# Optimization experiments

Hardware: AMD Instinct MI355X
Metric: run time of the kernel (lower is better)

The kernel has to match this reference:

```python
import jax, jax.numpy as jnp
import numpy as np

N = 10000
E = 320000


def spmm(edge_row, edge_col, edge_val, h):
    # out[i] = sum_{e: row[e]==i} val[e] * h[col[e]]  (sparse adjacency @ h)
    msgs = edge_val[:, None] * h[edge_col]          # [E, d]
    return jax.ops.segment_sum(msgs, edge_row, num_segments=N)


def setup_inputs() -> dict:
    key = jax.random.key(0)
    ks = jax.random.split(key, 8)
    x = jax.random.normal(ks[0], (N, 128), dtype=jnp.float32)
    edge_row = jax.random.randint(ks[1], (E,), 0, N, dtype=jnp.int32)
    edge_col = jax.random.randint(ks[2], (E,), 0, N, dtype=jnp.int32)
    edge_val = jax.random.uniform(ks[3], (E,), dtype=jnp.float32)
    # Xavier-uniform-ish init as in the torch module: U(-1/sqrt(fan_out), 1/sqrt(fan_out))
    def w(k, fi, fo):
        s = 1.0 / np.sqrt(fo)
        return jax.random.uniform(k, (fi, fo), minval=-s, maxval=s, dtype=jnp.float32)
    W0 = w(ks[4], 128, 128)
    W1 = w(ks[5], 128, 128)
    W2 = w(ks[6], 128, 64)
    Wb = w(ks[7], 64, 64)
    return {"x": x, "edge_row": edge_row, "edge_col": edge_col, "edge_val": edge_val,
            "W0": W0, "W1": W1, "W2": W2, "Wb": Wb}


def reference(x, edge_row, edge_col, edge_val, W0, W1, W2, Wb):
    h = x
    for W in (W0, W1, W2):
        h = jax.nn.elu(spmm(edge_row, edge_col, edge_val, h @ W))
        # dropout is inactive in eval mode (training=False)
    S = (Wb + Wb.T) * 0.5                          # symmetric [d, d]
    out = jax.nn.sigmoid(h @ (S @ h.T))            # [N, N]
    return out
```

## Files before the change

### kernel.cpp

```cpp
#include <hip/hip_runtime.h>
#include <hip/hip_bf16.h>
#include <math.h>

typedef short short8 __attribute__((ext_vector_type(8)));
typedef short short4v __attribute__((ext_vector_type(4)));
typedef float f32x4 __attribute__((ext_vector_type(4)));

__device__ inline void bsplit(float x, short& h, short& l) {
    __hip_bfloat16 hb = __float2bfloat16(x);
    float hf = __bfloat162float(hb);
    __hip_bfloat16 lb = __float2bfloat16(x - hf);
    h = *reinterpret_cast<short*>(&hb);
    l = *reinterpret_cast<short*>(&lb);
}


__global__ void zero_i32(int* __restrict__ p, int n) {
    int i = blockIdx.x * blockDim.x + threadIdx.x;
    if (i < n) p[i] = 0;
}

__global__ void hist_kernel(const int* __restrict__ row, int* __restrict__ hist, int E) {
    int i = blockIdx.x * blockDim.x + threadIdx.x;
    if (i < E) atomicAdd(&hist[row[i]], 1);
}

__global__ void scan_kernel(const int* __restrict__ hist, int* __restrict__ rowptr,
                            int* __restrict__ cursor, int n) {
    __shared__ int wsum[16];
    __shared__ int carry_s;
    int tid = threadIdx.x, lane = tid & 63, wid = tid >> 6;
    if (tid == 0) { carry_s = 0; rowptr[0] = 0; }
    __syncthreads();
    for (int base = 0; base < n; base += 1024) {
        int idx = base + tid;
        int v = (idx < n) ? hist[idx] : 0;
        int x = v;
#pragma unroll
        for (int d = 1; d < 64; d <<= 1) {
            int t = __shfl_up(x, d, 64);
            if (lane >= d) x += t;
        }
        if (lane == 63) wsum[wid] = x;
        __syncthreads();
        if (wid == 0) {
            int s = (lane < 16) ? wsum[lane] : 0;
#pragma unroll
            for (int d = 1; d < 16; d <<= 1) {
                int t = __shfl_up(s, d, 64);
                if (lane >= d) s += t;
            }
            if (lane < 16) wsum[lane] = s;
        }
        __syncthreads();
        int woff = (wid > 0) ? wsum[wid - 1] : 0;
        int inc = x + woff + carry_s;
        if (idx < n) {
            rowptr[idx + 1] = inc;
            cursor[idx] = inc - v;
        }
        __syncthreads();
        if (tid == 1023) carry_s = inc;
        __syncthreads();
    }
}

__global__ void scatter_kernel(const int* __restrict__ row, const int* __restrict__ col,
                               const float* __restrict__ val, int* __restrict__ cursor,
                               int* __restrict__ colsort, float* __restrict__ valsort, int E) {
    int i = blockIdx.x * blockDim.x + threadIdx.x;
    if (i < E) {
        int r = row[i];
        int p = atomicAdd(&cursor[r], 1);
        colsort[p] = col[i];
        valsort[p] = val[i];
    }
}

template <int K, int M>
__global__ void gemm_layer(const float* __restrict__ A, const float* __restrict__ W,
                           float* __restrict__ out, int n) {
    __shared__ float a[8 * K];
    int j = threadIdx.x;
    int row0 = blockIdx.x * 8;
    constexpr int K4 = K / 4;
    for (int idx = j; idx < 8 * K4; idx += M) {
        int r = idx / K4, k4 = idx % K4;
        float4 v = make_float4(0.f, 0.f, 0.f, 0.f);
        if (row0 + r < n) v = *reinterpret_cast<const float4*>(A + (long)(row0 + r) * K + k4 * 4);
        *reinterpret_cast<float4*>(a + r * K + k4 * 4) = v;
    }
    __syncthreads();
    float acc[8] = {0, 0, 0, 0, 0, 0, 0, 0};
#pragma unroll 8
    for (int k = 0; k < K; k++) {
        float w = W[k * M + j];
#pragma unroll
        for (int r = 0; r < 8; r++) acc[r] += a[r * K + k] * w;
    }
#pragma unroll
    for (int r = 0; r < 8; r++) {
        if (row0 + r < n) out[(long)(row0 + r) * M + j] = acc[r];
    }
}

template <int D>
__global__ void spmm_elu_v2(const int* __restrict__ rowptr, const int* __restrict__ cols,
                            const float* __restrict__ vals, const float* __restrict__ hw,
                            float* __restrict__ out, int n) {
    constexpr int LPR = D / 4;
    constexpr int EPI = 64 / LPR;
    int wave = (blockIdx.x * blockDim.x + threadIdx.x) >> 6;
    int lane = threadIdx.x & 63;
    if (wave >= n) return;
    int sub = lane % LPR, grp = lane / LPR;
    int s = rowptr[wave], e = rowptr[wave + 1];
    float ax = 0.f, ay = 0.f, az = 0.f, aw = 0.f;
    int pe = s + grp;
    int c = 0; float v = 0.f;
    if (pe < e) { c = cols[pe]; v = vals[pe]; }
    for (int p = s; p < e; p += EPI) {
        int pn = p + EPI + grp;
        int cn = 0; float vn = 0.f;
        if (pn < e) { cn = cols[pn]; vn = vals[pn]; }
        float4 h4 = *reinterpret_cast<const float4*>(hw + (long)c * D + sub * 4);
        ax += v * h4.x; ay += v * h4.y; az += v * h4.z; aw += v * h4.w;
        c = cn; v = vn;
    }
#pragma unroll
    for (int m = LPR; m < 64; m <<= 1) {
        ax += __shfl_xor(ax, m, 64);
        ay += __shfl_xor(ay, m, 64);
        az += __shfl_xor(az, m, 64);
        aw += __shfl_xor(aw, m, 64);
    }
    if (grp == 0) {
        float4 o;
        o.x = ax > 0.f ? ax : (__expf(ax) - 1.f);
        o.y = ay > 0.f ? ay : (__expf(ay) - 1.f);
        o.z = az > 0.f ? az : (__expf(az) - 1.f);
        o.w = aw > 0.f ? aw : (__expf(aw) - 1.f);
        *reinterpret_cast<float4*>(out + (long)wave * D + sub * 4) = o;
    }
}

__global__ void spmm_fused3(const int* __restrict__ rowptr, const int* __restrict__ cols,
                            const float* __restrict__ vals, const float* __restrict__ hw,
                            const float* __restrict__ S,
                            short* __restrict__ Hh, short* __restrict__ Hl,
                            short* __restrict__ Th, short* __restrict__ Tl, int n) {
    constexpr int D = 64, LPR = 16, EPI = 4;
    int wave = (blockIdx.x * blockDim.x + threadIdx.x) >> 6;
    int lane = threadIdx.x & 63;
    if (wave >= n) return;
    int sub = lane % LPR, grp = lane / LPR;
    int s = rowptr[wave], e = rowptr[wave + 1];
    float ax = 0.f, ay = 0.f, az = 0.f, aw = 0.f;
    int pe = s + grp;
    int c = 0; float v = 0.f;
    if (pe < e) { c = cols[pe]; v = vals[pe]; }
    for (int p = s; p < e; p += EPI) {
        int pn = p + EPI + grp;
        int cn = 0; float vn = 0.f;
        if (pn < e) { cn = cols[pn]; vn = vals[pn]; }
        float4 h4 = *reinterpret_cast<const float4*>(hw + (long)c * D + sub * 4);
        ax += v * h4.x; ay += v * h4.y; az += v * h4.z; aw += v * h4.w;
        c = cn; v = vn;
    }
#pragma unroll
    for (int m = LPR; m < 64; m <<= 1) {
        ax += __shfl_xor(ax, m, 64);
        ay += __shfl_xor(ay, m, 64);
        az += __shfl_xor(az, m, 64);
        aw += __shfl_xor(aw, m, 64);
    }
    float4 o;
    o.x = ax > 0.f ? ax : (__expf(ax) - 1.f);
    o.y = ay > 0.f ? ay : (__expf(ay) - 1.f);
    o.z = az > 0.f ? az : (__expf(az) - 1.f);
    o.w = aw > 0.f ? aw : (__expf(aw) - 1.f);

    if (grp == 0) {
        short4v hs, ls;
        short t0, t1, t2, t3, u0, u1, u2, u3;
        bsplit(o.x, t0, u0);
        bsplit(o.y, t1, u1);
        bsplit(o.z, t2, u2);
        bsplit(o.w, t3, u3);
        hs[0] = t0; hs[1] = t1; hs[2] = t2; hs[3] = t3;
        ls[0] = u0; ls[1] = u1; ls[2] = u2; ls[3] = u3;
        *reinterpret_cast<short4v*>(Hh + (long)wave * D + sub * 4) = hs;
        *reinterpret_cast<short4v*>(Hl + (long)wave * D + sub * 4) = ls;
    }

    float t = 0.f;
#pragma unroll
    for (int k = 0; k < 64; k++) {
        float hk;
        switch (k & 3) {
            case 0: hk = __shfl(o.x, k >> 2, 64); break;
            case 1: hk = __shfl(o.y, k >> 2, 64); break;
            case 2: hk = __shfl(o.z, k >> 2, 64); break;
            default: hk = __shfl(o.w, k >> 2, 64); break;
        }
        t += hk * S[k * 64 + lane];
    }
    short th, tl;
    bsplit(t, th, tl);
    Th[(long)wave * 64 + lane] = th;
    Tl[(long)wave * 64 + lane] = tl;
}

__global__ void sym_kernel(const float* __restrict__ Wb, float* __restrict__ S) {
    int i = blockIdx.x * blockDim.x + threadIdx.x;
    if (i < 64 * 64) {
        int r = i >> 6, c = i & 63;
        S[i] = 0.5f * (Wb[r * 64 + c] + Wb[c * 64 + r]);
    }
}

__global__ void pad_zero(short* __restrict__ Th, short* __restrict__ Tl,
                         short* __restrict__ Hh, short* __restrict__ Hl,
                         int startRow, int padRows) {
    int i = blockIdx.x * blockDim.x + threadIdx.x;
    int tot = padRows * 64;
    if (i < tot) {
        long off = (long)startRow * 64 + i;
        Th[off] = 0; Tl[off] = 0; Hh[off] = 0; Hl[off] = 0;
    }
}

__global__ __launch_bounds__(256, 2) void final_mfma(
    const short* __restrict__ Th, const short* __restrict__ Tl,
    const short* __restrict__ Hh, const short* __restrict__ Hl,
    float* __restrict__ out, int n, int G, int ypx) {
    int bid = blockIdx.x;
    int xcd = bid & 7;
    int s4 = bid >> 3;
    int by = xcd * ypx + s4 % ypx;
    int bx = s4 / ypx;
    if (by >= G) return;

    int tid = threadIdx.x;
    int wave = tid >> 6, lane = tid & 63;
    int row0 = by * 128 + (wave >> 1) * 64;
    int col0 = bx * 128 + (wave & 1) * 64;
    int lrow = lane & 15;
    int koff = (lane >> 4) * 8;

    const short* ThB = Th + (long)(row0 + lrow) * 64 + koff;
    const short* TlB = Tl + (long)(row0 + lrow) * 64 + koff;
    const short* HhB = Hh + (long)(col0 + lrow) * 64 + koff;
    const short* HlB = Hl + (long)(col0 + lrow) * 64 + koff;

    f32x4 acc[4][4];
#pragma unroll
    for (int r = 0; r < 4; r++)
#pragma unroll
        for (int c = 0; c < 4; c++) acc[r][c] = (f32x4){0.f, 0.f, 0.f, 0.f};

#pragma unroll
    for (int ks = 0; ks < 2; ks++) {
        int kb = ks * 32;
        short8 ah[4], al[4];
#pragma unroll
        for (int r = 0; r < 4; r++) ah[r] = *reinterpret_cast<const short8*>(ThB + (long)(r * 16) * 64 + kb);
#pragma unroll
        for (int r = 0; r < 4; r++) al[r] = *reinterpret_cast<const short8*>(TlB + (long)(r * 16) * 64 + kb);

#pragma unroll
        for (int c = 0; c < 4; c++) {
            short8 bh = *reinterpret_cast<const short8*>(HhB + (long)(c * 16) * 64 + kb);
            short8 bl = *reinterpret_cast<const short8*>(HlB + (long)(c * 16) * 64 + kb);
#pragma unroll
            for (int r = 0; r < 4; r++)
                acc[r][c] = __builtin_amdgcn_mfma_f32_16x16x32_bf16(ah[r], bh, acc[r][c], 0, 0, 0);
#pragma unroll
            for (int r = 0; r < 4; r++)
                acc[r][c] = __builtin_amdgcn_mfma_f32_16x16x32_bf16(ah[r], bl, acc[r][c], 0, 0, 0);
#pragma unroll
            for (int r = 0; r < 4; r++)
                acc[r][c] = __builtin_amdgcn_mfma_f32_16x16x32_bf16(al[r], bh, acc[r][c], 0, 0, 0);
        }
    }

    int orow = (lane >> 4) * 4;
    bool full = (row0 + 64 <= n) && (col0 + 64 <= n);
    if (full) {
#pragma unroll
        for (int r = 0; r < 4; r++) {
#pragma unroll
            for (int q = 0; q < 4; q++) {
                long base = (long)(row0 + r * 16 + orow + q) * n + col0 + lrow;
#pragma unroll
                for (int c = 0; c < 4; c++) {
                    float x = acc[r][c][q];
                    __builtin_nontemporal_store(__builtin_amdgcn_rcpf(1.f + __expf(-x)),
                                                out + base + c * 16);
                }
            }
        }
    } else {
#pragma unroll
        for (int r = 0; r < 4; r++) {
#pragma unroll
            for (int q = 0; q < 4; q++) {
                int i = row0 + r * 16 + orow + q;
                if (i < n) {
#pragma unroll
                    for (int c = 0; c < 4; c++) {
                        int j = col0 + c * 16 + lrow;
                        if (j < n) {
                            float x = acc[r][c][q];
                            __builtin_nontemporal_store(__builtin_amdgcn_rcpf(1.f + __expf(-x)),
                                                        out + (long)i * n + j);
                        }
                    }
                }
            }
        }
    }
}

extern "C" void kernel_launch(void* const* d_in, const int* in_sizes, int n_in,
                              void* d_out, int out_size, void* d_ws, size_t ws_size,
                              hipStream_t stream) {
    const float* x    = (const float*)d_in[0];
    const int*   erow = (const int*)d_in[1];
    const int*   ecol = (const int*)d_in[2];
    const float* eval = (const float*)d_in[3];
    const float* W0   = (const float*)d_in[4];
    const float* W1   = (const float*)d_in[5];
    const float* W2   = (const float*)d_in[6];
    const float* Wb   = (const float*)d_in[7];
    float* out = (float*)d_out;

    int N = in_sizes[0] / 128;
    int E = in_sizes[1];
    int G = (N + 127) / 128;
    int Npad = G * 128;

    char* w = (char*)d_ws;
    size_t off = 0;
    auto alloc = [&](size_t bytes) -> void* {
        void* p = w + off;
        off += (bytes + 255) & ~(size_t)255;
        return p;
    };
    float* bufA    = (float*)alloc((size_t)N * 128 * 4);
    float* bufB    = (float*)alloc((size_t)N * 128 * 4);
    float* S       = (float*)alloc(64 * 64 * 4);
    int*   colsort = (int*)alloc((size_t)E * 4);
    float* valsort = (float*)alloc((size_t)E * 4);
    int*   rowptr  = (int*)alloc((size_t)(N + 1) * 4);
    int*   cursor  = (int*)alloc((size_t)N * 4);
    int*   hist    = (int*)alloc((size_t)N * 4);
    short* Th      = (short*)alloc((size_t)Npad * 64 * 2);
    short* Tl      = (short*)alloc((size_t)Npad * 64 * 2);
    short* Hh      = (short*)alloc((size_t)Npad * 64 * 2);
    short* Hl      = (short*)alloc((size_t)Npad * 64 * 2);

    zero_i32<<<(N + 255) / 256, 256, 0, stream>>>(hist, N);
    hist_kernel<<<(E + 255) / 256, 256, 0, stream>>>(erow, hist, E);
    scan_kernel<<<1, 1024, 0, stream>>>(hist, rowptr, cursor, N);
    scatter_kernel<<<(E + 255) / 256, 256, 0, stream>>>(erow, ecol, eval, cursor, colsort, valsort, E);

    int gb8 = (N + 7) / 8;
    int spmmG = (N + 3) / 4;
    sym_kernel<<<16, 256, 0, stream>>>(Wb, S);
    gemm_layer<128, 128><<<gb8, 128, 0, stream>>>(x, W0, bufB, N);
    spmm_elu_v2<128><<<spmmG, 256, 0, stream>>>(rowptr, colsort, valsort, bufB, bufA, N);
    gemm_layer<128, 128><<<gb8, 128, 0, stream>>>(bufA, W1, bufB, N);
    spmm_elu_v2<128><<<spmmG, 256, 0, stream>>>(rowptr, colsort, valsort, bufB, bufA, N);
    gemm_layer<128, 64><<<gb8, 64, 0, stream>>>(bufA, W2, bufB, N);
    spmm_fused3<<<spmmG, 256, 0, stream>>>(rowptr, colsort, valsort, bufB, S, Hh, Hl, Th, Tl, N);

    int padRows = Npad - N;
    if (padRows > 0)
        pad_zero<<<(padRows * 64 + 255) / 256, 256, 0, stream>>>(Th, Tl, Hh, Hl, N, padRows);

    int ypx = (G + 7) / 8;
    int nwg = 8 * ypx * G;
    final_mfma<<<nwg, 256, 0, stream>>>(Th, Tl, Hh, Hl, out, N, G, ypx);
}
```

Baseline: 293.5 us.

## Enlarge final MFMA tile to 256x256 and parallelize the row-pointer scan

The final sigmoid(T·Hᵀ) kernel now uses 512-thread blocks covering a 256x256 output tile. Each wave computes a 64x128 sub-tile with 32 accumulators instead of 16, which raises operand reuse and cuts the number of workgroups. The single-block serial prefix scan over row histograms is replaced by a three-kernel multi-block scan: partial sums, a scan of the block sums, then a final pass. The larger tile raises register pressure and may lower occupancy. Padding grows to a multiple of 256 rows.

```diff
diff --git a/kernel.cpp b/kernel.cpp
--- a/kernel.cpp
+++ b/kernel.cpp
@@ -25,44 +25,55 @@
     if (i < E) atomicAdd(&hist[row[i]], 1);
 }
 
-__global__ void scan_kernel(const int* __restrict__ hist, int* __restrict__ rowptr,
-                            int* __restrict__ cursor, int n) {
-    __shared__ int wsum[16];
-    __shared__ int carry_s;
+__global__ __launch_bounds__(256) void scan_partial(const int* __restrict__ hist,
+                                                    int* __restrict__ bsum, int n) {
+    __shared__ int ws_[4];
     int tid = threadIdx.x, lane = tid & 63, wid = tid >> 6;
-    if (tid == 0) { carry_s = 0; rowptr[0] = 0; }
+    int idx = blockIdx.x * 256 + tid;
+    int x = (idx < n) ? hist[idx] : 0;
+#pragma unroll
+    for (int m = 1; m < 64; m <<= 1) x += __shfl_xor(x, m, 64);
+    if (lane == 0) ws_[wid] = x;
     __syncthreads();
-    for (int base = 0; base < n; base += 1024) {
-        int idx = base + tid;
-        int v = (idx < n) ? hist[idx] : 0;
-        int x = v;
-#pragma unroll
-        for (int d = 1; d < 64; d <<= 1) {
-            int t = __shfl_up(x, d, 64);
-            if (lane >= d) x += t;
-        }
-        if (lane == 63) wsum[wid] = x;
-        __syncthreads();
-        if (wid == 0) {
-            int s = (lane < 16) ? wsum[lane] : 0;
-#pragma unroll
-            for (int d = 1; d < 16; d <<= 1) {
-                int t = __shfl_up(s, d, 64);
-                if (lane >= d) s += t;
-            }
-            if (lane < 16) wsum[lane] = s;
-        }
-        __syncthreads();
-        int woff = (wid > 0) ? wsum[wid - 1] : 0;
-        int inc = x + woff + carry_s;
-        if (idx < n) {
-            rowptr[idx + 1] = inc;
-            cursor[idx] = inc - v;
-        }
-        __syncthreads();
-        if (tid == 1023) carry_s = inc;
-        __syncthreads();
-    }
+    if (tid == 0) bsum[blockIdx.x] = ws_[0] + ws_[1] + ws_[2] + ws_[3];
+}
+
+__global__ void scan_bsums(int* __restrict__ bsum, int nb) {
+    int lane = threadIdx.x & 63;
+    int x = (lane < nb) ? bsum[lane] : 0;
+#pragma unroll
+    for (int d = 1; d < 64; d <<= 1) {
+        int t = __shfl_up(x, d, 64);
+        if (lane >= d) x += t;
+    }
+    if (lane < nb) bsum[lane] = x;
+}
+
+__global__ __launch_bounds__(256) void scan_final(const int* __restrict__ hist,
+                                                  const int* __restrict__ bsum,
+                                                  int* __restrict__ rowptr,
+                                                  int* __restrict__ cursor, int n) {
+    __shared__ int wsum[4];
+    int tid = threadIdx.x, lane = tid & 63, wid = tid >> 6;
+    int b = blockIdx.x;
+    int idx = b * 256 + tid;
+    int v = (idx < n) ? hist[idx] : 0;
+    int x = v;
+#pragma unroll
+    for (int d = 1; d < 64; d <<= 1) {
+        int t = __shfl_up(x, d, 64);
+        if (lane >= d) x += t;
+    }
+    if (lane == 63) wsum[wid] = x;
+    __syncthreads();
+    int add = (b > 0) ? bsum[b - 1] : 0;
+    for (int w_ = 0; w_ < wid; w_++) add += wsum[w_];
+    int inc = x + add;
+    if (idx < n) {
+        rowptr[idx + 1] = inc;
+        cursor[idx] = inc - v;
+    }
+    if (b == 0 && tid == 0) rowptr[0] = 0;
 }
 
 __global__ void scatter_kernel(const int* __restrict__ row, const int* __restrict__ col,
@@ -230,7 +241,7 @@
     }
 }
 
-__global__ __launch_bounds__(256, 2) void final_mfma(
+__global__ __launch_bounds__(512, 2) void final_mfma(
     const short* __restrict__ Th, const short* __restrict__ Tl,
     const short* __restrict__ Hh, const short* __restrict__ Hl,
     float* __restrict__ out, int n, int G, int ypx) {
@@ -243,8 +254,9 @@
 
     int tid = threadIdx.x;
     int wave = tid >> 6, lane = tid & 63;
-    int row0 = by * 128 + (wave >> 1) * 64;
-    int col0 = bx * 128 + (wave & 1) * 64;
+    int wr = wave >> 1, wc = wave & 1;
+    int row0 = by * 256 + wr * 64;
+    int col0 = bx * 256 + wc * 128;
     int lrow = lane & 15;
     int koff = (lane >> 4) * 8;
 
@@ -253,11 +265,11 @@
     const short* HhB = Hh + (long)(col0 + lrow) * 64 + koff;
     const short* HlB = Hl + (long)(col0 + lrow) * 64 + koff;
 
-    f32x4 acc[4][4];
+    f32x4 acc[4][8];
 #pragma unroll
     for (int r = 0; r < 4; r++)
 #pragma unroll
-        for (int c = 0; c < 4; c++) acc[r][c] = (f32x4){0.f, 0.f, 0.f, 0.f};
+        for (int c = 0; c < 8; c++) acc[r][c] = (f32x4){0.f, 0.f, 0.f, 0.f};
 
 #pragma unroll
     for (int ks = 0; ks < 2; ks++) {
@@ -269,7 +281,7 @@
         for (int r = 0; r < 4; r++) al[r] = *reinterpret_cast<const short8*>(TlB + (long)(r * 16) * 64 + kb);
 
 #pragma unroll
-        for (int c = 0; c < 4; c++) {
+        for (int c = 0; c < 8; c++) {
             short8 bh = *reinterpret_cast<const short8*>(HhB + (long)(c * 16) * 64 + kb);
             short8 bl = *reinterpret_cast<const short8*>(HlB + (long)(c * 16) * 64 + kb);
 #pragma unroll
@@ -285,7 +297,7 @@
     }
 
     int orow = (lane >> 4) * 4;
-    bool full = (row0 + 64 <= n) && (col0 + 64 <= n);
+    bool full = (row0 + 64 <= n) && (col0 + 128 <= n);
     if (full) {
 #pragma unroll
         for (int r = 0; r < 4; r++) {
@@ -293,7 +305,7 @@
             for (int q = 0; q < 4; q++) {
                 long base = (long)(row0 + r * 16 + orow + q) * n + col0 + lrow;
 #pragma unroll
-                for (int c = 0; c < 4; c++) {
+                for (int c = 0; c < 8; c++) {
                     float x = acc[r][c][q];
                     __builtin_nontemporal_store(__builtin_amdgcn_rcpf(1.f + __expf(-x)),
                                                 out + base + c * 16);
@@ -308,7 +320,7 @@
                 int i = row0 + r * 16 + orow + q;
                 if (i < n) {
 #pragma unroll
-                    for (int c = 0; c < 4; c++) {
+                    for (int c = 0; c < 8; c++) {
                         int j = col0 + c * 16 + lrow;
                         if (j < n) {
                             float x = acc[r][c][q];
@@ -337,8 +349,8 @@
 
     int N = in_sizes[0] / 128;
     int E = in_sizes[1];
-    int G = (N + 127) / 128;
-    int Npad = G * 128;
+    int G = (N + 255) / 256;
+    int Npad = G * 256;
 
     char* w = (char*)d_ws;
     size_t off = 0;
@@ -355,14 +367,18 @@
     int*   rowptr  = (int*)alloc((size_t)(N + 1) * 4);
     int*   cursor  = (int*)alloc((size_t)N * 4);
     int*   hist    = (int*)alloc((size_t)N * 4);
+    int*   bsum    = (int*)alloc(64 * 4);
     short* Th      = (short*)alloc((size_t)Npad * 64 * 2);
     short* Tl      = (short*)alloc((size_t)Npad * 64 * 2);
     short* Hh      = (short*)alloc((size_t)Npad * 64 * 2);
     short* Hl      = (short*)alloc((size_t)Npad * 64 * 2);
 
+    int nb = (N + 255) / 256;
     zero_i32<<<(N + 255) / 256, 256, 0, stream>>>(hist, N);
     hist_kernel<<<(E + 255) / 256, 256, 0, stream>>>(erow, hist, E);
-    scan_kernel<<<1, 1024, 0, stream>>>(hist, rowptr, cursor, N);
+    scan_partial<<<nb, 256, 0, stream>>>(hist, bsum, N);
+    scan_bsums<<<1, 64, 0, stream>>>(bsum, nb);
+    scan_final<<<nb, 256, 0, stream>>>(hist, bsum, rowptr, cursor, N);
     scatter_kernel<<<(E + 255) / 256, 256, 0, stream>>>(erow, ecol, eval, cursor, colsort, valsort, E);
 
     int gb8 = (N + 7) / 8;
@@ -381,5 +397,5 @@
 
     int ypx = (G + 7) / 8;
     int nwg = 8 * ypx * G;
-    final_mfma<<<nwg, 256, 0, stream>>>(Th, Tl, Hh, Hl, out, N, G, ypx);
-}
+    final_mfma<<<nwg, 512, 0, stream>>>(Th, Tl, Hh, Hl, out, N, G, ypx);
+}
```

New measurement: 311.0 us. 1.06x slower.
